# Kernel optimization log

Measured on AMD Instinct MI355X. Metric: run time of the kernel, lower is better.

The kernel has to match this reference:

```python
import jax, jax.numpy as jnp
import numpy as np

UNITS = 2048

def _cat_complex(Wr, Wi):
    # real-matrix representation of complex matmul: [[Wr, -Wi], [Wi, Wr]]
    top = jnp.concatenate([Wr, -Wi], axis=-1)
    bot = jnp.concatenate([Wi, Wr], axis=-1)
    return jnp.concatenate([top, bot], axis=0)

def _hard_sigmoid(x):
    return jnp.clip(0.2 * x + 0.5, 0.0, 1.0)

def setup_inputs() -> dict:
    key = jax.random.key(0)
    ks = jax.random.split(key, 8)
    B, IN2, U3 = 1024, 4096, 3 * UNITS
    s_in = 1.0 / np.sqrt(IN2)
    s_h = 1.0 / np.sqrt(2 * UNITS)
    return {
        "inputs": jax.random.normal(ks[0], (B, IN2), jnp.float32),
        "h_tm1": jax.random.normal(ks[1], (B, 2 * UNITS), jnp.float32),
        "real_kernel": jax.random.normal(ks[2], (IN2 // 2, U3), jnp.float32) * s_in,
        "imaginary_kernel": jax.random.normal(ks[3], (IN2 // 2, U3), jnp.float32) * s_in,
        "real_recurrent_kernel": jax.random.normal(ks[4], (UNITS, U3), jnp.float32) * s_h,
        "imaginary_recurrent_kernel": jax.random.normal(ks[5], (UNITS, U3), jnp.float32) * s_h,
        "real_bias": jax.random.normal(ks[6], (U3,), jnp.float32) * 0.01,
        "imaginary_bias": jax.random.normal(ks[7], (U3,), jnp.float32) * 0.01,
    }

def reference(inputs, h_tm1, real_kernel, imaginary_kernel,
              real_recurrent_kernel, imaginary_recurrent_kernel,
              real_bias, imaginary_bias):
    u = UNITS
    # per-gate complex kernels in real [[Wr,-Wi],[Wi,Wr]] form
    Kz = _cat_complex(real_kernel[:, :u], imaginary_kernel[:, :u])
    Kr = _cat_complex(real_kernel[:, u:2 * u], imaginary_kernel[:, u:2 * u])
    Kh = _cat_complex(real_kernel[:, 2 * u:], imaginary_kernel[:, 2 * u:])
    Rz = _cat_complex(real_recurrent_kernel[:, :u], imaginary_recurrent_kernel[:, :u])
    Rr = _cat_complex(real_recurrent_kernel[:, u:2 * u], imaginary_recurrent_kernel[:, u:2 * u])
    Rh = _cat_complex(real_recurrent_kernel[:, 2 * u:], imaginary_recurrent_kernel[:, 2 * u:])
    bz = jnp.concatenate([real_bias[:u], imaginary_bias[:u]])
    br = jnp.concatenate([real_bias[u:2 * u], imaginary_bias[u:2 * u]])
    bh = jnp.concatenate([real_bias[2 * u:], imaginary_bias[2 * u:]])
    # implementation=1, reset_after=False, no dropout
    x_z = inputs @ Kz + bz
    x_r = inputs @ Kr + br
    x_h = inputs @ Kh + bh
    z = _hard_sigmoid(x_z + h_tm1 @ Rz)
    r = _hard_sigmoid(x_r + h_tm1 @ Rr)
    hh = jnp.tanh(x_h + (r * h_tm1) @ Rh)
    h = z * h_tm1 + (1.0 - z) * hh
    return h
```

## Files before the change

kernel.cpp:

```cpp
#include <hip/hip_runtime.h>

typedef _Float16 half8  __attribute__((ext_vector_type(8)));
typedef _Float16 half4v __attribute__((ext_vector_type(4)));
typedef _Float16 half2v __attribute__((ext_vector_type(2)));
typedef float    float4v __attribute__((ext_vector_type(4)));

__device__ __forceinline__ float hsig(float x) {
  return fminf(fmaxf(fmaf(x, 0.2f, 0.5f), 0.0f), 1.0f);
}

__global__ __launch_bounds__(256) void cvt_pair(const float* __restrict__ src,
                                                _Float16* __restrict__ d1,
                                                _Float16* __restrict__ d2) {
  int i = blockIdx.x * blockDim.x + threadIdx.x;
  int base = i * 4;
  int j = base & 4095;
  float s = (j < 2048) ? -1.0f : 1.0f;
  float4 v = *(const float4*)&src[base];
  half4v h1 = {(_Float16)v.x, (_Float16)v.y, (_Float16)v.z, (_Float16)v.w};
  half4v h2 = {(_Float16)(s * v.x), (_Float16)(s * v.y), (_Float16)(s * v.z), (_Float16)(s * v.w)};
  *(half4v*)&d1[base] = h1;
  *(half4v*)&d2[base] = h2;
}

__global__ __launch_bounds__(256) void transpose_cast(
    const float* __restrict__ s0, const float* __restrict__ s1,
    const float* __restrict__ s2, const float* __restrict__ s3,
    _Float16* __restrict__ d0, _Float16* __restrict__ d1m,
    _Float16* __restrict__ d2m, _Float16* __restrict__ d3m)
{
  __shared__ float tile[64][65];
  const float* srcs[4] = {s0, s1, s2, s3};
  _Float16*    dsts[4] = {d0, d1m, d2m, d3m};
  const float* src = srcs[blockIdx.z];
  _Float16*    dst = dsts[blockIdx.z];

  const int tid = threadIdx.x;
  const int k0 = blockIdx.x * 64;
  const int j0 = blockIdx.y * 64;

  const int tx = tid & 63, ty = tid >> 6;
#pragma unroll
  for (int r = 0; r < 64; r += 4)
    tile[r + ty][tx] = src[(size_t)(k0 + r + ty) * 6144 + j0 + tx];
  __syncthreads();

  const int txk = (tid & 31) * 2;
  const int tyn = tid >> 5;
#pragma unroll
  for (int r = 0; r < 64; r += 8) {
    int jl = r + tyn;
    half2v p = {(_Float16)tile[txk][jl], (_Float16)tile[txk + 1][jl]};
    *(half2v*)&dst[(size_t)(j0 + jl) * 2048 + k0 + txk] = p;
  }
}

__global__ __launch_bounds__(256) void rgate(const _Float16* __restrict__ xacc,
                                             const float* __restrict__ h,
                                             _Float16* __restrict__ A1r,
                                             _Float16* __restrict__ A2r) {
  int i = blockIdx.x * blockDim.x + threadIdx.x;
  int base = i * 4;
  int m = base >> 12;
  int j = base & 4095;
  float s = (j < 2048) ? -1.0f : 1.0f;
  half4v rp = *(const half4v*)&xacc[(size_t)m * 12288 + 4096 + j];
  float4 hv = *(const float4*)&h[base];
  float p0 = hsig((float)rp[0]) * hv.x;
  float p1 = hsig((float)rp[1]) * hv.y;
  float p2 = hsig((float)rp[2]) * hv.z;
  float p3 = hsig((float)rp[3]) * hv.w;
  half4v o1 = {(_Float16)p0, (_Float16)p1, (_Float16)p2, (_Float16)p3};
  half4v o2 = {(_Float16)(s * p0), (_Float16)(s * p1), (_Float16)(s * p2), (_Float16)(s * p3)};
  *(half4v*)&A1r[base] = o1;
  *(half4v*)&A2r[base] = o2;
}

__global__ __launch_bounds__(256) void combine(const _Float16* __restrict__ xacc,
                                               const _Float16* __restrict__ P0,
                                               const _Float16* __restrict__ P1,
                                               const float* __restrict__ h,
                                               float* __restrict__ out) {
  int i = blockIdx.x * blockDim.x + threadIdx.x;
  int base = i * 4;
  int m = base >> 12;
  int j = base & 4095;
  half4v zv = *(const half4v*)&xacc[(size_t)m * 12288 + j];
  half4v xh = *(const half4v*)&xacc[(size_t)m * 12288 + 8192 + j];
  half4v p0 = *(const half4v*)&P0[base];
  half4v p1 = *(const half4v*)&P1[base];
  float4 hv = *(const float4*)&h[base];
  float4 o;
  {
    float z = hsig((float)zv[0]); float t = tanhf((float)xh[0] + (float)p0[0] + (float)p1[0]);
    o.x = z * hv.x + (1.0f - z) * t;
  }
  {
    float z = hsig((float)zv[1]); float t = tanhf((float)xh[1] + (float)p0[1] + (float)p1[1]);
    o.y = z * hv.y + (1.0f - z) * t;
  }
  {
    float z = hsig((float)zv[2]); float t = tanhf((float)xh[2] + (float)p0[2] + (float)p1[2]);
    o.z = z * hv.z + (1.0f - z) * t;
  }
  {
    float z = hsig((float)zv[3]); float t = tanhf((float)xh[3] + (float)p0[3] + (float)p1[3]);
    o.w = z * hv.w + (1.0f - z) * t;
  }
  *(float4*)&out[base] = o;
}

template<int FINAL>
__global__ __launch_bounds__(256, 3) void gemm_big(
    const _Float16* __restrict__ Ax1, const _Float16* __restrict__ Ax2,
    const _Float16* __restrict__ Ah1, const _Float16* __restrict__ Ah2,
    const _Float16* __restrict__ WKr, const _Float16* __restrict__ WKi,
    const _Float16* __restrict__ WRr, const _Float16* __restrict__ WRi,
    _Float16* __restrict__ xacc,
    _Float16* __restrict__ P0, _Float16* __restrict__ P1,
    const float* __restrict__ rbias, const float* __restrict__ ibias)
{
  __shared__ __align__(16) _Float16 lds[16384];
  const int tid  = threadIdx.x;
  const int lane = tid & 63;
  const int wave = tid >> 6;
  const int quad = lane >> 4;
  const int r16  = lane & 15;
  const int wm = (wave >> 1) * 64;
  const int wn = (wave & 1) * 64;
  const int mbase = blockIdx.y * 128;
  const int nbase = blockIdx.x * 128;

  const int  gate   = nbase >> 12;
  const bool hi     = (nbase & 2048) != 0;
  const int  jprime = nbase & 2047;

  int nph;
  const _Float16* pA[4];
  const _Float16* pB[4];
  if (FINAL) {
    nph = 1;
    const _Float16* Ax = hi ? Ax2 : Ax1;
    const _Float16* BL = hi ? WKi : WKr;
    const _Float16* BH = hi ? WKr : WKi;
    if (blockIdx.z == 0) {
      pA[0] = Ax + (size_t)mbase * 4096;
      pB[0] = BL + (size_t)jprime * 2048;
    } else {
      pA[0] = Ax + (size_t)mbase * 4096 + 2048;
      pB[0] = BH + (size_t)jprime * 2048;
    }
  } else {
    const size_t browK = (size_t)(gate * 2048 + jprime) * 2048;
    const _Float16* Ax = hi ? Ax2 : Ax1;
    const _Float16* KL = hi ? WKi : WKr;
    const _Float16* KH = hi ? WKr : WKi;
    pA[0] = Ax + (size_t)mbase * 4096;      pB[0] = KL + browK;
    pA[1] = pA[0] + 2048;                   pB[1] = KH + browK;
    if (gate < 2) {
      nph = 4;
      const _Float16* Ah = hi ? Ah2 : Ah1;
      const _Float16* RL = hi ? WRi : WRr;
      const _Float16* RH = hi ? WRr : WRi;
      pA[2] = Ah + (size_t)mbase * 4096;    pB[2] = RL + browK;
      pA[3] = pA[2] + 2048;                 pB[3] = RH + browK;
    } else {
      nph = 2;
    }
  }

  float4v acc[4][4];
#pragma unroll
  for (int i = 0; i < 4; ++i)
#pragma unroll
    for (int j = 0; j < 4; ++j) acc[i][j] = (float4v){0.f, 0.f, 0.f, 0.f};

  int offA[4], offB[4], ldsA[4], ldsB[4];
#pragma unroll
  for (int i = 0; i < 4; ++i) {
    int c = i * 256 + tid;
    int row = c >> 3;
    int sw = (c & 7) ^ (row & 7);
    offA[i] = row * 4096 + sw * 8;
    offB[i] = row * 2048 + sw * 8;
    ldsA[i] = c * 8;
    ldsB[i] = 8192 + c * 8;
  }

#pragma unroll 1
  for (int p = 0; p < 4; ++p) {
    if (p >= nph) break;
    const _Float16* Ab = pA[p];
    const _Float16* Bb = pB[p];
#pragma unroll 1
    for (int it = 0; it < 32; ++it) {
#pragma unroll
      for (int i = 0; i < 4; ++i)
        __builtin_amdgcn_global_load_lds(
            (__attribute__((address_space(1))) void*)(Ab + offA[i]),
            (__attribute__((address_space(3))) void*)&lds[ldsA[i]], 16, 0, 0);
#pragma unroll
      for (int i = 0; i < 4; ++i)
        __builtin_amdgcn_global_load_lds(
            (__attribute__((address_space(1))) void*)(Bb + offB[i]),
            (__attribute__((address_space(3))) void*)&lds[ldsB[i]], 16, 0, 0);
      Ab += 64;
      Bb += 64;
      __syncthreads();
#pragma unroll
      for (int ks = 0; ks < 2; ++ks) {
        half8 af[4], bf[4];
        int akg = ks * 4 + quad;
#pragma unroll
        for (int t = 0; t < 4; ++t) {
          int arow = wm + t * 16 + r16;
          af[t] = *(const half8*)&lds[(arow * 8 + (akg ^ (arow & 7))) * 8];
          int brow = wn + t * 16 + r16;
          bf[t] = *(const half8*)&lds[8192 + (brow * 8 + (akg ^ (brow & 7))) * 8];
        }
#pragma unroll
        for (int mt = 0; mt < 4; ++mt)
#pragma unroll
          for (int nt = 0; nt < 4; ++nt)
            acc[mt][nt] = __builtin_amdgcn_mfma_f32_16x16x32_f16(af[mt], bf[nt], acc[mt][nt], 0, 0, 0);
      }
      __syncthreads();
    }
  }

  const int mrow0 = mbase + wm + quad * 4;
  const int ncol0 = nbase + wn + r16;
  if (!FINAL) {
#pragma unroll
    for (int nt = 0; nt < 4; ++nt) {
      int n = ncol0 + nt * 16;
      int g = n >> 12, j = n & 4095;
      float b = (j < 2048) ? rbias[g * 2048 + j] : ibias[g * 2048 + j - 2048];
#pragma unroll
      for (int mt = 0; mt < 4; ++mt)
#pragma unroll
        for (int e = 0; e < 4; ++e) {
          int m = mrow0 + mt * 16 + e;
          xacc[(size_t)m * 12288 + n] = (_Float16)(acc[mt][nt][e] + b);
        }
    }
  } else {
    _Float16* P = blockIdx.z ? P1 : P0;
#pragma unroll
    for (int nt = 0; nt < 4; ++nt) {
      int n = ncol0 + nt * 16;
#pragma unroll
      for (int mt = 0; mt < 4; ++mt)
#pragma unroll
        for (int e = 0; e < 4; ++e) {
          int m = mrow0 + mt * 16 + e;
          P[(size_t)m * 4096 + n] = (_Float16)acc[mt][nt][e];
        }
    }
  }
}

extern "C" void kernel_launch(void* const* d_in, const int* in_sizes, int n_in,
                              void* d_out, int out_size, void* d_ws, size_t ws_size,
                              hipStream_t stream) {
  const float* inputs = (const float*)d_in[0];
  const float* h_tm1  = (const float*)d_in[1];
  const float* rk     = (const float*)d_in[2];
  const float* ik     = (const float*)d_in[3];
  const float* rrk    = (const float*)d_in[4];
  const float* irk    = (const float*)d_in[5];
  const float* rb     = (const float*)d_in[6];
  const float* ib     = (const float*)d_in[7];
  float* out = (float*)d_out;

  char* ws = (char*)d_ws;
  _Float16* WrK  = (_Float16*)(ws + 0);
  _Float16* WiK  = (_Float16*)(ws + 25165824);
  _Float16* WrR  = (_Float16*)(ws + 50331648);
  _Float16* WiR  = (_Float16*)(ws + 75497472);
  _Float16* A1x  = (_Float16*)(ws + 100663296);
  _Float16* A2x  = (_Float16*)(ws + 109051904);
  _Float16* A1h  = (_Float16*)(ws + 117440512);
  _Float16* A2h  = (_Float16*)(ws + 125829120);
  _Float16* xacc = (_Float16*)(ws + 134217728);
  _Float16* A1r  = A1x;
  _Float16* A2r  = A2x;
  _Float16* P0   = A1h;
  _Float16* P1   = A2h;

  cvt_pair<<<4096, 256, 0, stream>>>(inputs, A1x, A2x);
  cvt_pair<<<4096, 256, 0, stream>>>(h_tm1, A1h, A2h);
  transpose_cast<<<dim3(32, 96, 4), 256, 0, stream>>>(rk, ik, rrk, irk, WrK, WiK, WrR, WiR);
  gemm_big<0><<<dim3(96, 8), 256, 0, stream>>>(A1x, A2x, A1h, A2h, WrK, WiK, WrR, WiR,
                                               xacc, nullptr, nullptr, rb, ib);
  rgate<<<4096, 256, 0, stream>>>(xacc, h_tm1, A1r, A2r);
  gemm_big<1><<<dim3(32, 8, 2), 256, 0, stream>>>(A1r, A2r, nullptr, nullptr,
                                                  WrR + (size_t)4096 * 2048,
                                                  WiR + (size_t)4096 * 2048,
                                                  nullptr, nullptr, nullptr, P0, P1,
                                                  nullptr, nullptr);
  combine<<<4096, 256, 0, stream>>>(xacc, P0, P1, h_tm1, out);
}
```

Before: 512.9 us.

## Fuse reset gate into GEMM epilogue, remap blocks across XCDs, vectorize prep kernels

```diff
diff --git a/kernel.cpp b/kernel.cpp
--- a/kernel.cpp
+++ b/kernel.cpp
@@ -2,17 +2,20 @@
 
 typedef _Float16 half8  __attribute__((ext_vector_type(8)));
 typedef _Float16 half4v __attribute__((ext_vector_type(4)));
-typedef _Float16 half2v __attribute__((ext_vector_type(2)));
 typedef float    float4v __attribute__((ext_vector_type(4)));
 
 __device__ __forceinline__ float hsig(float x) {
   return fminf(fmaxf(fmaf(x, 0.2f, 0.5f), 0.0f), 1.0f);
 }
 
-__global__ __launch_bounds__(256) void cvt_pair(const float* __restrict__ src,
-                                                _Float16* __restrict__ d1,
-                                                _Float16* __restrict__ d2) {
-  int i = blockIdx.x * blockDim.x + threadIdx.x;
+__global__ __launch_bounds__(256) void cvt_pair(const float* __restrict__ x,
+                                                const float* __restrict__ h,
+                                                _Float16* __restrict__ d1x, _Float16* __restrict__ d2x,
+                                                _Float16* __restrict__ d1h, _Float16* __restrict__ d2h) {
+  const float* src = blockIdx.y ? h : x;
+  _Float16* d1 = blockIdx.y ? d1h : d1x;
+  _Float16* d2 = blockIdx.y ? d2h : d2x;
+  int i = blockIdx.x * 256 + threadIdx.x;
   int base = i * 4;
   int j = base & 4095;
   float s = (j < 2048) ? -1.0f : 1.0f;
@@ -39,75 +42,28 @@
   const int k0 = blockIdx.x * 64;
   const int j0 = blockIdx.y * 64;
 
-  const int tx = tid & 63, ty = tid >> 6;
-#pragma unroll
-  for (int r = 0; r < 64; r += 4)
-    tile[r + ty][tx] = src[(size_t)(k0 + r + ty) * 6144 + j0 + tx];
+  const int rr = tid >> 4;
+  const int c4 = (tid & 15) * 4;
+#pragma unroll
+  for (int it = 0; it < 4; ++it) {
+    int row = it * 16 + rr;
+    float4 v = *(const float4*)&src[(size_t)(k0 + row) * 6144 + j0 + c4];
+    tile[row][c4]     = v.x;
+    tile[row][c4 + 1] = v.y;
+    tile[row][c4 + 2] = v.z;
+    tile[row][c4 + 3] = v.w;
+  }
   __syncthreads();
-
-  const int txk = (tid & 31) * 2;
-  const int tyn = tid >> 5;
-#pragma unroll
-  for (int r = 0; r < 64; r += 8) {
-    int jl = r + tyn;
-    half2v p = {(_Float16)tile[txk][jl], (_Float16)tile[txk + 1][jl]};
-    *(half2v*)&dst[(size_t)(j0 + jl) * 2048 + k0 + txk] = p;
-  }
-}
-
-__global__ __launch_bounds__(256) void rgate(const _Float16* __restrict__ xacc,
-                                             const float* __restrict__ h,
-                                             _Float16* __restrict__ A1r,
-                                             _Float16* __restrict__ A2r) {
-  int i = blockIdx.x * blockDim.x + threadIdx.x;
-  int base = i * 4;
-  int m = base >> 12;
-  int j = base & 4095;
-  float s = (j < 2048) ? -1.0f : 1.0f;
-  half4v rp = *(const half4v*)&xacc[(size_t)m * 12288 + 4096 + j];
-  float4 hv = *(const float4*)&h[base];
-  float p0 = hsig((float)rp[0]) * hv.x;
-  float p1 = hsig((float)rp[1]) * hv.y;
-  float p2 = hsig((float)rp[2]) * hv.z;
-  float p3 = hsig((float)rp[3]) * hv.w;
-  half4v o1 = {(_Float16)p0, (_Float16)p1, (_Float16)p2, (_Float16)p3};
-  half4v o2 = {(_Float16)(s * p0), (_Float16)(s * p1), (_Float16)(s * p2), (_Float16)(s * p3)};
-  *(half4v*)&A1r[base] = o1;
-  *(half4v*)&A2r[base] = o2;
-}
-
-__global__ __launch_bounds__(256) void combine(const _Float16* __restrict__ xacc,
-                                               const _Float16* __restrict__ P0,
-                                               const _Float16* __restrict__ P1,
-                                               const float* __restrict__ h,
-                                               float* __restrict__ out) {
-  int i = blockIdx.x * blockDim.x + threadIdx.x;
-  int base = i * 4;
-  int m = base >> 12;
-  int j = base & 4095;
-  half4v zv = *(const half4v*)&xacc[(size_t)m * 12288 + j];
-  half4v xh = *(const half4v*)&xacc[(size_t)m * 12288 + 8192 + j];
-  half4v p0 = *(const half4v*)&P0[base];
-  half4v p1 = *(const half4v*)&P1[base];
-  float4 hv = *(const float4*)&h[base];
-  float4 o;
-  {
-    float z = hsig((float)zv[0]); float t = tanhf((float)xh[0] + (float)p0[0] + (float)p1[0]);
-    o.x = z * hv.x + (1.0f - z) * t;
-  }
-  {
-    float z = hsig((float)zv[1]); float t = tanhf((float)xh[1] + (float)p0[1] + (float)p1[1]);
-    o.y = z * hv.y + (1.0f - z) * t;
-  }
-  {
-    float z = hsig((float)zv[2]); float t = tanhf((float)xh[2] + (float)p0[2] + (float)p1[2]);
-    o.z = z * hv.z + (1.0f - z) * t;
-  }
-  {
-    float z = hsig((float)zv[3]); float t = tanhf((float)xh[3] + (float)p0[3] + (float)p1[3]);
-    o.w = z * hv.w + (1.0f - z) * t;
-  }
-  *(float4*)&out[base] = o;
+  const int k8 = (tid & 7) * 8;
+  const int jb = tid >> 3;
+#pragma unroll
+  for (int it = 0; it < 2; ++it) {
+    int jl = it * 32 + jb;
+    half8 hv;
+#pragma unroll
+    for (int i = 0; i < 8; ++i) hv[i] = (_Float16)tile[k8 + i][jl];
+    *(half8*)&dst[(size_t)(j0 + jl) * 2048 + k0 + k8] = hv;
+  }
 }
 
 template<int FINAL>
@@ -118,7 +74,9 @@
     const _Float16* __restrict__ WRr, const _Float16* __restrict__ WRi,
     _Float16* __restrict__ xacc,
     _Float16* __restrict__ P0, _Float16* __restrict__ P1,
-    const float* __restrict__ rbias, const float* __restrict__ ibias)
+    const float* __restrict__ rbias, const float* __restrict__ ibias,
+    const float* __restrict__ hfull,
+    _Float16* __restrict__ A1r, _Float16* __restrict__ A2r)
 {
   __shared__ __align__(16) _Float16 lds[16384];
   const int tid  = threadIdx.x;
@@ -128,8 +86,23 @@
   const int r16  = lane & 15;
   const int wm = (wave >> 1) * 64;
   const int wn = (wave & 1) * 64;
-  const int mbase = blockIdx.y * 128;
-  const int nbase = blockIdx.x * 128;
+
+  int mbase, nbase;
+  if (FINAL) {
+    mbase = blockIdx.y * 128;
+    nbase = blockIdx.x * 128;
+  } else {
+    const int wgid = blockIdx.y * 96 + blockIdx.x;
+    const int xcd = wgid & 7;
+    const int a   = wgid >> 3;
+    const int by  = a / 12;
+    const int p   = a - by * 12;
+    const signed char LUT[12] = {0, 1, 8, 2, 9, 3, 4, 10, 5, 11, 6, 7};
+    const int bxl = LUT[p];
+    const int bx  = bxl * 8 + xcd;
+    mbase = by * 128;
+    nbase = bx * 128;
+  }
 
   const int  gate   = nbase >> 12;
   const bool hi     = (nbase & 2048) != 0;
@@ -231,18 +204,37 @@
   const int mrow0 = mbase + wm + quad * 4;
   const int ncol0 = nbase + wn + r16;
   if (!FINAL) {
-#pragma unroll
-    for (int nt = 0; nt < 4; ++nt) {
-      int n = ncol0 + nt * 16;
-      int g = n >> 12, j = n & 4095;
-      float b = (j < 2048) ? rbias[g * 2048 + j] : ibias[g * 2048 + j - 2048];
-#pragma unroll
-      for (int mt = 0; mt < 4; ++mt)
-#pragma unroll
-        for (int e = 0; e < 4; ++e) {
-          int m = mrow0 + mt * 16 + e;
-          xacc[(size_t)m * 12288 + n] = (_Float16)(acc[mt][nt][e] + b);
-        }
+    if (gate == 1) {
+#pragma unroll
+      for (int nt = 0; nt < 4; ++nt) {
+        int n = ncol0 + nt * 16;
+        int j = n & 4095;
+        float b = (j < 2048) ? rbias[2048 + j] : ibias[j];
+        float s = (j < 2048) ? -1.0f : 1.0f;
+#pragma unroll
+        for (int mt = 0; mt < 4; ++mt)
+#pragma unroll
+          for (int e = 0; e < 4; ++e) {
+            int m = mrow0 + mt * 16 + e;
+            float pv = hsig(acc[mt][nt][e] + b) * hfull[(size_t)m * 4096 + j];
+            A1r[(size_t)m * 4096 + j] = (_Float16)pv;
+            A2r[(size_t)m * 4096 + j] = (_Float16)(s * pv);
+          }
+      }
+    } else {
+#pragma unroll
+      for (int nt = 0; nt < 4; ++nt) {
+        int n = ncol0 + nt * 16;
+        int g = n >> 12, j = n & 4095;
+        float b = (j < 2048) ? rbias[g * 2048 + j] : ibias[g * 2048 + j - 2048];
+#pragma unroll
+        for (int mt = 0; mt < 4; ++mt)
+#pragma unroll
+          for (int e = 0; e < 4; ++e) {
+            int m = mrow0 + mt * 16 + e;
+            xacc[(size_t)m * 12288 + n] = (_Float16)(acc[mt][nt][e] + b);
+          }
+      }
     }
   } else {
     _Float16* P = blockIdx.z ? P1 : P0;
@@ -258,6 +250,40 @@
         }
     }
   }
+}
+
+__global__ __launch_bounds__(256) void combine(const _Float16* __restrict__ xacc,
+                                               const _Float16* __restrict__ P0,
+                                               const _Float16* __restrict__ P1,
+                                               const float* __restrict__ h,
+                                               float* __restrict__ out) {
+  int i = blockIdx.x * 256 + threadIdx.x;
+  int base = i * 4;
+  int m = base >> 12;
+  int j = base & 4095;
+  half4v zv = *(const half4v*)&xacc[(size_t)m * 12288 + j];
+  half4v xh = *(const half4v*)&xacc[(size_t)m * 12288 + 8192 + j];
+  half4v p0 = *(const half4v*)&P0[base];
+  half4v p1 = *(const half4v*)&P1[base];
+  float4 hv = *(const float4*)&h[base];
+  float4 o;
+  {
+    float z = hsig((float)zv[0]); float t = tanhf((float)xh[0] + (float)p0[0] + (float)p1[0]);
+    o.x = z * hv.x + (1.0f - z) * t;
+  }
+  {
+    float z = hsig((float)zv[1]); float t = tanhf((float)xh[1] + (float)p0[1] + (float)p1[1]);
+    o.y = z * hv.y + (1.0f - z) * t;
+  }
+  {
+    float z = hsig((float)zv[2]); float t = tanhf((float)xh[2] + (float)p0[2] + (float)p1[2]);
+    o.z = z * hv.z + (1.0f - z) * t;
+  }
+  {
+    float z = hsig((float)zv[3]); float t = tanhf((float)xh[3] + (float)p0[3] + (float)p1[3]);
+    o.w = z * hv.w + (1.0f - z) * t;
+  }
+  *(float4*)&out[base] = o;
 }
 
 extern "C" void kernel_launch(void* const* d_in, const int* in_sizes, int n_in,
@@ -283,21 +309,20 @@
   _Float16* A1h  = (_Float16*)(ws + 117440512);
   _Float16* A2h  = (_Float16*)(ws + 125829120);
   _Float16* xacc = (_Float16*)(ws + 134217728);
-  _Float16* A1r  = A1x;
-  _Float16* A2r  = A2x;
+  _Float16* A1r  = (_Float16*)(ws + 159383552);
+  _Float16* A2r  = (_Float16*)(ws + 167772160);
   _Float16* P0   = A1h;
   _Float16* P1   = A2h;
 
-  cvt_pair<<<4096, 256, 0, stream>>>(inputs, A1x, A2x);
-  cvt_pair<<<4096, 256, 0, stream>>>(h_tm1, A1h, A2h);
+  cvt_pair<<<dim3(4096, 2), 256, 0, stream>>>(inputs, h_tm1, A1x, A2x, A1h, A2h);
   transpose_cast<<<dim3(32, 96, 4), 256, 0, stream>>>(rk, ik, rrk, irk, WrK, WiK, WrR, WiR);
   gemm_big<0><<<dim3(96, 8), 256, 0, stream>>>(A1x, A2x, A1h, A2h, WrK, WiK, WrR, WiR,
-                                               xacc, nullptr, nullptr, rb, ib);
-  rgate<<<4096, 256, 0, stream>>>(xacc, h_tm1, A1r, A2r);
+                                               xacc, nullptr, nullptr, rb, ib,
+                                               h_tm1, A1r, A2r);
   gemm_big<1><<<dim3(32, 8, 2), 256, 0, stream>>>(A1r, A2r, nullptr, nullptr,
                                                   WrR + (size_t)4096 * 2048,
                                                   WiR + (size_t)4096 * 2048,
                                                   nullptr, nullptr, nullptr, P0, P1,
-                                                  nullptr, nullptr);
+                                                  nullptr, nullptr, nullptr, nullptr, nullptr);
   combine<<<4096, 256, 0, stream>>>(xacc, P0, P1, h_tm1, out);
 }
```

Measured after the change: 491.0 us. -4.3%, faster.
